# Optimization experiments

Hardware: AMD Instinct MI355X
Metric: run time of the kernel (lower is better)

## Reference

```python
import jax, jax.numpy as jnp
import numpy as np

B, L, IN_DIM = 4, 2048, 1024
H, D = 16, 64
OUT_DIM = 1024


def setup_inputs() -> dict:
    key = jax.random.key(0)
    k1, k2, k3 = jax.random.split(key, 3)
    inputs = jax.random.normal(k1, (B, L, IN_DIM), dtype=jnp.float32)
    # nn.Linear weight init scale ~ 1/sqrt(fan_in); keep values moderate
    W_qkv = jax.random.normal(k2, (IN_DIM, 3 * H * D), dtype=jnp.float32) * (IN_DIM ** -0.5)
    W_out = jax.random.normal(k3, (H * D, OUT_DIM), dtype=jnp.float32) * ((H * D) ** -0.5)
    return {"inputs": inputs, "W_qkv": W_qkv, "W_out": W_out}


def reference(inputs, W_qkv, W_out):
    b, l, _ = inputs.shape
    qkv = inputs @ W_qkv                      # [B, L, 3*H*D]
    q, k, v = jnp.split(qkv, 3, axis=-1)
    q = q.reshape(b, l, H, D)
    k = k.reshape(b, l, H, D)
    v = v.reshape(b, l, H, D)
    score = jnp.einsum('bihd,bjhd->bijh', q, k) / (D ** 0.5)  # [B, L, L, H]
    # sequence_mask(arange(1..L)) == lower-triangular causal mask
    mask = jnp.tril(jnp.ones((l, l), dtype=score.dtype))[None, :, :, None]
    masked_score = score * mask + 1e30 * (mask - 1.0)
    wmat = jax.nn.softmax(masked_score, axis=2)
    out = jnp.einsum('bijh,bjhd->bihd', wmat, v).reshape(b, l, H * D)
    return out @ W_out
```

## Files before the change

### kernel.cpp

```cpp
#include <hip/hip_runtime.h>

#define DEVI __device__ __forceinline__

typedef __attribute__((ext_vector_type(8))) short bh8;
typedef __attribute__((ext_vector_type(4))) float f32x4;

static constexpr int Bsz  = 4;
static constexpr int Lseq = 2048;
static constexpr int INDIM = 1024;
static constexpr int NH = 16;
static constexpr int HD = 64;
static constexpr int QKVN = 3 * NH * HD;
static constexpr int OUTD = 1024;
static constexpr int Mrows = Bsz * Lseq;

DEVI unsigned short f2bf(float f) {
    unsigned u = __float_as_uint(f);
    u = u + 0x7fffu + ((u >> 16) & 1u);
    return (unsigned short)(u >> 16);
}

DEVI void gl2lds16(const unsigned short* g, unsigned short* l) {
    __builtin_amdgcn_global_load_lds(
        (const __attribute__((address_space(1))) void*)g,
        (__attribute__((address_space(3))) void*)l, 16, 0, 0);
}

static constexpr int CV_BLKS = Mrows * INDIM / 8 / 256;
static constexpr int TQ_BLKS = (QKVN / 64) * (INDIM / 64);
static constexpr int TO_BLKS = (OUTD / 64) * ((NH * HD) / 64);

__global__ __launch_bounds__(256) void prep_fused(
    const float* __restrict__ X, unsigned short* __restrict__ Xb,
    const float* __restrict__ Wqkv, unsigned short* __restrict__ WqkvT,
    const float* __restrict__ Wout, unsigned short* __restrict__ WoutT) {
    __shared__ unsigned short t[64][65];
    int bid = blockIdx.x, tid = threadIdx.x;
    if (bid < CV_BLKS) {
        int i = bid * 256 + tid;
        const f32x4* p = (const f32x4*)(X + (size_t)i * 8);
        f32x4 a = p[0], b = p[1];
        bh8 o;
        o[0] = (short)f2bf(a[0]); o[1] = (short)f2bf(a[1]);
        o[2] = (short)f2bf(a[2]); o[3] = (short)f2bf(a[3]);
        o[4] = (short)f2bf(b[0]); o[5] = (short)f2bf(b[1]);
        o[6] = (short)f2bf(b[2]); o[7] = (short)f2bf(b[3]);
        *(bh8*)(Xb + (size_t)i * 8) = o;
        return;
    }
    const float* W; unsigned short* Wt; int K, N, n0, k0;
    if (bid < CV_BLKS + TQ_BLKS) {
        int tb = bid - CV_BLKS;
        K = INDIM; N = QKVN;
        n0 = (tb % (QKVN / 64)) * 64; k0 = (tb / (QKVN / 64)) * 64;
        W = Wqkv; Wt = WqkvT;
    } else {
        int tb = bid - CV_BLKS - TQ_BLKS;
        K = NH * HD; N = OUTD;
        n0 = (tb % (OUTD / 64)) * 64; k0 = (tb / (OUTD / 64)) * 64;
        W = Wout; Wt = WoutT;
    }
#pragma unroll
    for (int i = 0; i < 16; ++i) {
        int idx = tid + i * 256;
        int r = idx >> 6, c = idx & 63;
        t[r][c] = f2bf(W[(size_t)(k0 + r) * N + (n0 + c)]);
    }
    __syncthreads();
#pragma unroll
    for (int i = 0; i < 16; ++i) {
        int idx = tid + i * 256;
        int r = idx >> 6, c = idx & 63;
        Wt[(size_t)(n0 + r) * K + (k0 + c)] = t[c][r];
    }
}

template <int MODE>
__global__ __launch_bounds__(256) void gemm_bt(
    const unsigned short* __restrict__ A, const unsigned short* __restrict__ Bt,
    float* __restrict__ Cf, unsigned short* __restrict__ Qg,
    unsigned short* __restrict__ Kg, unsigned short* __restrict__ Vg,
    int K, int ntn, int cpx) {
    __shared__ unsigned short Al[2][128 * 64];
    __shared__ unsigned short Bl[2][128 * 64];
    int tid = threadIdx.x;
    int lane = tid & 63, wave = tid >> 6;
    int bid = blockIdx.x;
    int swz = (bid & 7) * cpx + (bid >> 3);
    int mt = swz / ntn, nt_ = swz % ntn;
    int m0 = mt * 128, n0 = nt_ * 128;
    int wm = (wave >> 1) * 64, wn = (wave & 1) * 64;

    int srow = tid >> 3;
    int scol = ((tid & 7) ^ (srow & 7)) * 8;
    const unsigned short* Ags = A + (size_t)(m0 + srow) * K + scol;
    const unsigned short* Bgs = Bt + (size_t)(n0 + srow) * K + scol;
    int wofs = wave * 512;

    f32x4 acc[4][4] = {};
    int cl = lane & 15, kq = (lane >> 4) * 8;

    int nt = K >> 6;
    auto stage = [&](int t, int buf) {
        int kof = t * 64;
#pragma unroll
        for (int i = 0; i < 4; ++i) {
            gl2lds16(Ags + (size_t)(32 * i) * K + kof, &Al[buf][0] + 32 * i * 64 + wofs);
            gl2lds16(Bgs + (size_t)(32 * i) * K + kof, &Bl[buf][0] + 32 * i * 64 + wofs);
        }
    };

    stage(0, 0);
    __syncthreads();

    int cur = 0;
    for (int t = 0; t < nt; ++t) {
        if (t + 1 < nt) stage(t + 1, cur ^ 1);
        bh8 af[4][2], bf[4][2];
#pragma unroll
        for (int mi = 0; mi < 4; ++mi) {
            int ar = wm + mi * 16 + cl, as = (ar & 7) << 3;
#pragma unroll
            for (int ks = 0; ks < 2; ++ks)
                af[mi][ks] = *(const bh8*)(&Al[cur][0] + ar * 64 + ((ks * 32 + kq) ^ as));
        }
#pragma unroll
        for (int nj = 0; nj < 4; ++nj) {
            int br = wn + nj * 16 + cl, bs = (br & 7) << 3;
#pragma unroll
            for (int ks = 0; ks < 2; ++ks)
                bf[nj][ks] = *(const bh8*)(&Bl[cur][0] + br * 64 + ((ks * 32 + kq) ^ bs));
        }
#pragma unroll
        for (int ks = 0; ks < 2; ++ks)
#pragma unroll
            for (int mi = 0; mi < 4; ++mi)
#pragma unroll
                for (int nj = 0; nj < 4; ++nj)
                    acc[mi][nj] = __builtin_amdgcn_mfma_f32_16x16x32_bf16(
                        af[mi][ks], bf[nj][ks], acc[mi][nj], 0, 0, 0);
        if (t + 1 < nt) __syncthreads();
        cur ^= 1;
    }

    int rb = (lane >> 4) * 4;
#pragma unroll
    for (int mi = 0; mi < 4; ++mi) {
#pragma unroll
        for (int nj = 0; nj < 4; ++nj) {
#pragma unroll
            for (int r = 0; r < 4; ++r) {
                int gm = m0 + wm + mi * 16 + rb + r;
                int gn = n0 + wn + nj * 16 + cl;
                float v = acc[mi][nj][r];
                if (MODE == 0) {
                    int b = gm >> 11, ls = gm & 2047;
                    int sel = gn >> 10, h = (gn >> 6) & 15, d = gn & 63;
                    if (sel == 0)
                        Qg[((size_t)(b * NH + h) * Lseq + ls) * HD + d] = f2bf(v * 0.125f);
                    else if (sel == 1)
                        Kg[((size_t)(b * NH + h) * Lseq + ls) * HD + d] = f2bf(v);
                    else
                        Vg[((size_t)(b * NH + h) * HD + d) * Lseq + ls] = f2bf(v);
                } else {
                    Cf[(size_t)gm * OUTD + gn] = v;
                }
            }
        }
    }
}

__global__ __launch_bounds__(256) void attn_causal(
    const unsigned short* __restrict__ Qg, const unsigned short* __restrict__ Kg,
    const unsigned short* __restrict__ Vt, unsigned short* __restrict__ Og) {
    __shared__ unsigned short Kl[64 * 64];
    __shared__ unsigned short Vl[64 * 64];
    __shared__ unsigned short Pl[4][16 * 72];
    int tid = threadIdx.x, wave = tid >> 6, lane = tid & 63;
    int bid = blockIdx.x;
    int xcd = bid & 7, slot = bid >> 3;
    int p = slot & 15;
    int bh = ((slot >> 4) << 3) | xcd;
    int b = bh >> 4, h = bh & 15;
    const unsigned short* Qp = Qg + (size_t)bh * Lseq * HD;
    const unsigned short* Kp = Kg + (size_t)bh * Lseq * HD;
    const unsigned short* Vp = Vt + (size_t)bh * HD * Lseq;
    int cl = lane & 15, kq = (lane >> 4) * 8, rb = (lane >> 4) * 4;
    unsigned short* Pw = &Pl[wave][0];

    int srow = tid >> 2;
    int sc0 = (tid & 3) * 16;
    int ssw = (srow & 7) << 3;

    bh8 ones;
#pragma unroll
    for (int i = 0; i < 8; ++i) ones[i] = (short)0x3F80;

    for (int pass = 0; pass < 2; ++pass) {
        int pt = pass ? (31 - p) : p;
        int q0 = pt * 64 + wave * 16;

        bh8 qf0 = *(const bh8*)(Qp + (size_t)(q0 + cl) * HD + kq);
        bh8 qf1 = *(const bh8*)(Qp + (size_t)(q0 + cl) * HD + 32 + kq);

        f32x4 o[4] = {};
        f32x4 osum = {};

        int nblk = pt + 1;
        for (int j = 0; j < nblk; ++j) {
            int kv0 = j * 64;
            bool masked = (j == nblk - 1);
            const unsigned short* Ks = Kp + (size_t)(kv0 + srow) * HD;
            const unsigned short* Vs = Vp + (size_t)srow * Lseq + kv0;
            bh8 k0 = *(const bh8*)(Ks + sc0);
            bh8 k1 = *(const bh8*)(Ks + sc0 + 8);
            bh8 v0 = *(const bh8*)(Vs + sc0);
            bh8 v1 = *(const bh8*)(Vs + sc0 + 8);
            __syncthreads();
            *(bh8*)(Kl + srow * 64 + (sc0 ^ ssw)) = k0;
            *(bh8*)(Kl + srow * 64 + ((sc0 + 8) ^ ssw)) = k1;
            *(bh8*)(Vl + srow * 64 + (sc0 ^ ssw)) = v0;
            *(bh8*)(Vl + srow * 64 + ((sc0 + 8) ^ ssw)) = v1;
            __syncthreads();
            __builtin_amdgcn_s_setprio(1);
#pragma unroll
            for (int nb = 0; nb < 4; ++nb) {
                int row = nb * 16 + cl, rs = (row & 7) << 3;
                bh8 kf0 = *(const bh8*)(Kl + row * 64 + (kq ^ rs));
                bh8 kf1 = *(const bh8*)(Kl + row * 64 + ((kq + 32) ^ rs));
                f32x4 s = {};
                s = __builtin_amdgcn_mfma_f32_16x16x32_bf16(qf0, kf0, s, 0, 0, 0);
                s = __builtin_amdgcn_mfma_f32_16x16x32_bf16(qf1, kf1, s, 0, 0, 0);
                if (masked) {
                    int col = kv0 + nb * 16 + cl;
#pragma unroll
                    for (int r = 0; r < 4; ++r) {
                        float v = s[r];
                        if (col > q0 + rb + r) v = -3e30f;
                        Pw[(rb + r) * 72 + nb * 16 + cl] = f2bf(__expf(v));
                    }
                } else {
#pragma unroll
                    for (int r = 0; r < 4; ++r)
                        Pw[(rb + r) * 72 + nb * 16 + cl] = f2bf(__expf(s[r]));
                }
            }
            bh8 pa0 = *(const bh8*)(Pw + cl * 72 + kq);
            bh8 pa1 = *(const bh8*)(Pw + cl * 72 + 32 + kq);
#pragma unroll
            for (int db = 0; db < 4; ++db) {
                int dr = db * 16 + cl, ds = (dr & 7) << 3;
                bh8 vf0 = *(const bh8*)(Vl + dr * 64 + (kq ^ ds));
                bh8 vf1 = *(const bh8*)(Vl + dr * 64 + ((kq + 32) ^ ds));
                o[db] = __builtin_amdgcn_mfma_f32_16x16x32_bf16(pa0, vf0, o[db], 0, 0, 0);
                o[db] = __builtin_amdgcn_mfma_f32_16x16x32_bf16(pa1, vf1, o[db], 0, 0, 0);
            }
            osum = __builtin_amdgcn_mfma_f32_16x16x32_bf16(pa0, ones, osum, 0, 0, 0);
            osum = __builtin_amdgcn_mfma_f32_16x16x32_bf16(pa1, ones, osum, 0, 0, 0);
            __builtin_amdgcn_s_setprio(0);
        }
#pragma unroll
        for (int r = 0; r < 4; ++r) {
            float inv = 1.0f / osum[r];
            int row = q0 + rb + r;
            size_t obase = (size_t)(b * Lseq + row) * OUTD + h * HD;
#pragma unroll
            for (int db = 0; db < 4; ++db)
                Og[obase + db * 16 + cl] = f2bf(o[db][r] * inv);
        }
    }
}

extern "C" void kernel_launch(void* const* d_in, const int* in_sizes, int n_in,
                              void* d_out, int out_size, void* d_ws, size_t ws_size,
                              hipStream_t stream) {
    (void)in_sizes; (void)n_in; (void)out_size; (void)ws_size;
    const float* X    = (const float*)d_in[0];
    const float* Wqkv = (const float*)d_in[1];
    const float* Wout = (const float*)d_in[2];
    float* out = (float*)d_out;

    char* ws = (char*)d_ws;
    size_t off = 0;
    unsigned short* Xb    = (unsigned short*)(ws + off); off += (size_t)Mrows * INDIM * 2;
    unsigned short* WqkvT = (unsigned short*)(ws + off); off += (size_t)QKVN * INDIM * 2;
    unsigned short* WoutT = (unsigned short*)(ws + off); off += (size_t)OUTD * (NH * HD) * 2;
    unsigned short* Qg    = (unsigned short*)(ws + off); off += (size_t)Mrows * NH * HD * 2;
    unsigned short* Kg    = (unsigned short*)(ws + off); off += (size_t)Mrows * NH * HD * 2;
    unsigned short* Vtg   = (unsigned short*)(ws + off); off += (size_t)Mrows * NH * HD * 2;
    unsigned short* Ob    = (unsigned short*)(ws + off); off += (size_t)Mrows * NH * HD * 2;

    prep_fused<<<CV_BLKS + TQ_BLKS + TO_BLKS, 256, 0, stream>>>(
        X, Xb, Wqkv, WqkvT, Wout, WoutT);
    gemm_bt<0><<<(Mrows / 128) * (QKVN / 128), 256, 0, stream>>>(
        Xb, WqkvT, nullptr, Qg, Kg, Vtg, INDIM, QKVN / 128,
        (Mrows / 128) * (QKVN / 128) / 8);
    attn_causal<<<Bsz * NH * 16, 256, 0, stream>>>(Qg, Kg, Vtg, Ob);
    gemm_bt<1><<<(Mrows / 128) * (OUTD / 128), 256, 0, stream>>>(
        Ob, WoutT, out, nullptr, nullptr, nullptr, NH * HD, OUTD / 128,
        (Mrows / 128) * (OUTD / 128) / 8);
}
```

Baseline: 189.7 us.

## Double-buffer K/V tiles in attention and swizzle P scratch layout

```diff
diff --git a/kernel.cpp b/kernel.cpp
--- a/kernel.cpp
+++ b/kernel.cpp
@@ -173,9 +173,9 @@
 __global__ __launch_bounds__(256) void attn_causal(
     const unsigned short* __restrict__ Qg, const unsigned short* __restrict__ Kg,
     const unsigned short* __restrict__ Vt, unsigned short* __restrict__ Og) {
-    __shared__ unsigned short Kl[64 * 64];
-    __shared__ unsigned short Vl[64 * 64];
-    __shared__ unsigned short Pl[4][16 * 72];
+    __shared__ unsigned short Kl[2][64 * 64];
+    __shared__ unsigned short Vl[2][64 * 64];
+    __shared__ unsigned short Pl[4][16 * 64];
     int tid = threadIdx.x, wave = tid >> 6, lane = tid & 63;
     int bid = blockIdx.x;
     int xcd = bid & 7, slot = bid >> 3;
@@ -187,6 +187,7 @@
     const unsigned short* Vp = Vt + (size_t)bh * HD * Lseq;
     int cl = lane & 15, kq = (lane >> 4) * 8, rb = (lane >> 4) * 4;
     unsigned short* Pw = &Pl[wave][0];
+    int psw = (cl & 7) << 3;
 
     int srow = tid >> 2;
     int sc0 = (tid & 3) * 16;
@@ -207,27 +208,43 @@
         f32x4 osum = {};
 
         int nblk = pt + 1;
-        for (int j = 0; j < nblk; ++j) {
-            int kv0 = j * 64;
-            bool masked = (j == nblk - 1);
-            const unsigned short* Ks = Kp + (size_t)(kv0 + srow) * HD;
-            const unsigned short* Vs = Vp + (size_t)srow * Lseq + kv0;
+        {
+            const unsigned short* Ks = Kp + (size_t)srow * HD;
+            const unsigned short* Vs = Vp + (size_t)srow * Lseq;
             bh8 k0 = *(const bh8*)(Ks + sc0);
             bh8 k1 = *(const bh8*)(Ks + sc0 + 8);
             bh8 v0 = *(const bh8*)(Vs + sc0);
             bh8 v1 = *(const bh8*)(Vs + sc0 + 8);
             __syncthreads();
-            *(bh8*)(Kl + srow * 64 + (sc0 ^ ssw)) = k0;
-            *(bh8*)(Kl + srow * 64 + ((sc0 + 8) ^ ssw)) = k1;
-            *(bh8*)(Vl + srow * 64 + (sc0 ^ ssw)) = v0;
-            *(bh8*)(Vl + srow * 64 + ((sc0 + 8) ^ ssw)) = v1;
+            *(bh8*)(&Kl[0][0] + srow * 64 + (sc0 ^ ssw)) = k0;
+            *(bh8*)(&Kl[0][0] + srow * 64 + ((sc0 + 8) ^ ssw)) = k1;
+            *(bh8*)(&Vl[0][0] + srow * 64 + (sc0 ^ ssw)) = v0;
+            *(bh8*)(&Vl[0][0] + srow * 64 + ((sc0 + 8) ^ ssw)) = v1;
             __syncthreads();
+        }
+        int cur = 0;
+        for (int j = 0; j < nblk; ++j) {
+            int kv0 = j * 64;
+            bool masked = (j == nblk - 1);
+            bool pre = (j + 1 < nblk);
+            bh8 k0, k1, v0, v1;
+            if (pre) {
+                int kn = kv0 + 64;
+                const unsigned short* Ks = Kp + (size_t)(kn + srow) * HD;
+                const unsigned short* Vs = Vp + (size_t)srow * Lseq + kn;
+                k0 = *(const bh8*)(Ks + sc0);
+                k1 = *(const bh8*)(Ks + sc0 + 8);
+                v0 = *(const bh8*)(Vs + sc0);
+                v1 = *(const bh8*)(Vs + sc0 + 8);
+            }
             __builtin_amdgcn_s_setprio(1);
+            const unsigned short* Kc = &Kl[cur][0];
+            const unsigned short* Vc = &Vl[cur][0];
 #pragma unroll
             for (int nb = 0; nb < 4; ++nb) {
                 int row = nb * 16 + cl, rs = (row & 7) << 3;
-                bh8 kf0 = *(const bh8*)(Kl + row * 64 + (kq ^ rs));
-                bh8 kf1 = *(const bh8*)(Kl + row * 64 + ((kq + 32) ^ rs));
+                bh8 kf0 = *(const bh8*)(Kc + row * 64 + (kq ^ rs));
+                bh8 kf1 = *(const bh8*)(Kc + row * 64 + ((kq + 32) ^ rs));
                 f32x4 s = {};
                 s = __builtin_amdgcn_mfma_f32_16x16x32_bf16(qf0, kf0, s, 0, 0, 0);
                 s = __builtin_amdgcn_mfma_f32_16x16x32_bf16(qf1, kf1, s, 0, 0, 0);
@@ -237,27 +254,38 @@
                     for (int r = 0; r < 4; ++r) {
                         float v = s[r];
                         if (col > q0 + rb + r) v = -3e30f;
-                        Pw[(rb + r) * 72 + nb * 16 + cl] = f2bf(__expf(v));
+                        int rr = rb + r;
+                        Pw[rr * 64 + ((nb * 16 + cl) ^ ((rr & 7) << 3))] = f2bf(__expf(v));
                     }
                 } else {
 #pragma unroll
-                    for (int r = 0; r < 4; ++r)
-                        Pw[(rb + r) * 72 + nb * 16 + cl] = f2bf(__expf(s[r]));
+                    for (int r = 0; r < 4; ++r) {
+                        int rr = rb + r;
+                        Pw[rr * 64 + ((nb * 16 + cl) ^ ((rr & 7) << 3))] = f2bf(__expf(s[r]));
+                    }
                 }
             }
-            bh8 pa0 = *(const bh8*)(Pw + cl * 72 + kq);
-            bh8 pa1 = *(const bh8*)(Pw + cl * 72 + 32 + kq);
+            bh8 pa0 = *(const bh8*)(Pw + cl * 64 + (kq ^ psw));
+            bh8 pa1 = *(const bh8*)(Pw + cl * 64 + ((32 + kq) ^ psw));
 #pragma unroll
             for (int db = 0; db < 4; ++db) {
                 int dr = db * 16 + cl, ds = (dr & 7) << 3;
-                bh8 vf0 = *(const bh8*)(Vl + dr * 64 + (kq ^ ds));
-                bh8 vf1 = *(const bh8*)(Vl + dr * 64 + ((kq + 32) ^ ds));
+                bh8 vf0 = *(const bh8*)(Vc + dr * 64 + (kq ^ ds));
+                bh8 vf1 = *(const bh8*)(Vc + dr * 64 + ((kq + 32) ^ ds));
                 o[db] = __builtin_amdgcn_mfma_f32_16x16x32_bf16(pa0, vf0, o[db], 0, 0, 0);
                 o[db] = __builtin_amdgcn_mfma_f32_16x16x32_bf16(pa1, vf1, o[db], 0, 0, 0);
             }
             osum = __builtin_amdgcn_mfma_f32_16x16x32_bf16(pa0, ones, osum, 0, 0, 0);
             osum = __builtin_amdgcn_mfma_f32_16x16x32_bf16(pa1, ones, osum, 0, 0, 0);
             __builtin_amdgcn_s_setprio(0);
+            if (pre) {
+                *(bh8*)(&Kl[cur ^ 1][0] + srow * 64 + (sc0 ^ ssw)) = k0;
+                *(bh8*)(&Kl[cur ^ 1][0] + srow * 64 + ((sc0 + 8) ^ ssw)) = k1;
+                *(bh8*)(&Vl[cur ^ 1][0] + srow * 64 + (sc0 ^ ssw)) = v0;
+                *(bh8*)(&Vl[cur ^ 1][0] + srow * 64 + ((sc0 + 8) ^ ssw)) = v1;
+            }
+            __syncthreads();
+            cur ^= 1;
         }
 #pragma unroll
         for (int r = 0; r < 4; ++r) {
```

Result: slower. 198.1 us (+4.4%).
